# Optimization experiments

Measured on AMD Instinct MI355X. Metric: run time of the kernel, lower is better.

The kernel has to match this reference:

```python
import jax, jax.numpy as jnp
import numpy as np

N_NODES = 100000
N_EDGES = 1600000
N_FEAT = 64
HIDDEN = 16


def setup_inputs() -> dict:
    key = jax.random.key(0)
    ks = jax.random.split(key, 10)
    x = jax.random.normal(ks[0], (N_NODES, N_FEAT), dtype=jnp.float32)
    edge_index = jax.random.randint(ks[1], (2, N_EDGES), 0, N_NODES, dtype=jnp.int64)
    As = jax.random.normal(ks[2], (2, N_EDGES), dtype=jnp.float32)
    ws_weights = jax.random.normal(ks[3], (2,), dtype=jnp.float32)
    Wl1 = jax.random.normal(ks[4], (N_FEAT, HIDDEN), dtype=jnp.float32) / np.sqrt(N_FEAT)
    bl1 = jnp.zeros((HIDDEN,), dtype=jnp.float32)
    Wr1 = jax.random.normal(ks[5], (N_FEAT, HIDDEN), dtype=jnp.float32) / np.sqrt(N_FEAT)
    Wl2 = jax.random.normal(ks[6], (HIDDEN, 1), dtype=jnp.float32) / np.sqrt(HIDDEN)
    bl2 = jnp.zeros((1,), dtype=jnp.float32)
    Wr2 = jax.random.normal(ks[7], (HIDDEN, 1), dtype=jnp.float32) / np.sqrt(HIDDEN)
    return {"x": x, "edge_index": edge_index, "As": As, "ws_weights": ws_weights,
            "Wl1": Wl1, "bl1": bl1, "Wr1": Wr1, "Wl2": Wl2, "bl2": bl2, "Wr2": Wr2}


def reference(x, edge_index, As, ws_weights, Wl1, bl1, Wr1, Wl2, bl2, Wr2):
    # WeightedSumLayer: weighted sum of per-edge weight vectors
    ewm = jnp.einsum('m,me->e', ws_weights, As)  # [E]
    # edge mask (nonzero weighted sum keeps the edge); instead of slicing to a
    # data-dependent edge count, zero out masked messages (same aggregation).
    mask = (ewm != 0).astype(x.dtype)  # [E]
    src, dst = edge_index[0], edge_index[1]
    n = x.shape[0]

    # SAGEConv layer 1 (aggr='sum'): out = lin_l(sum_j x_j) + lin_r(x)
    msg1 = x[src] * mask[:, None]                             # [E, F]
    agg1 = jax.ops.segment_sum(msg1, dst, num_segments=n)     # [N, F]
    h = jax.nn.relu(agg1 @ Wl1 + bl1 + x @ Wr1)               # [N, H]

    # SAGEConv layer 2
    msg2 = h[src] * mask[:, None]                             # [E, H]
    agg2 = jax.ops.segment_sum(msg2, dst, num_segments=n)     # [N, H]
    out = agg2 @ Wl2 + bl2 + h @ Wr2                          # [N, 1]
    return out
```

## Files before the change

### kernel.cpp

```cpp
#include <hip/hip_runtime.h>
#include <hip/hip_bf16.h>

constexpr int NN = 100000;
constexpr int NE = 1600000;
constexpr int NF = 64;
constexpr int NH = 16;

constexpr int NPB  = 128;
constexpr int LB   = 7;
constexpr int NBKT = (NN + NPB - 1) / NPB;
constexpr int CAP  = 2560;
constexpr int TB   = 512;
constexpr int CHUNK = 8192;
constexpr int NBF   = (NE + CHUNK - 1) / CHUNK;
constexpr int NBLK_K1 = (NN + TB - 1) / TB;
constexpr int FD = NBKT + 1;

constexpr int SMEM_BYTES = CHUNK * 2 + NBKT * 4 + FD * 4 + TB * 4;

__device__ __forceinline__ float bf16_to_f32(unsigned short u) {
    return __uint_as_float(((unsigned int)u) << 16);
}
__device__ __forceinline__ unsigned short f32_to_bf16(float f) {
    __hip_bfloat16 hb = __float2bfloat16(f);
    return *reinterpret_cast<unsigned short*>(&hb);
}

__global__ __launch_bounds__(TB)
void k_fused(const float* __restrict__ x,
             const float* __restrict__ Wl1,
             const float* __restrict__ Wr1,
             unsigned short* __restrict__ p,
             float* __restrict__ r,
             const int* __restrict__ ei, const float* __restrict__ As,
             const float* __restrict__ ws,
             unsigned int* __restrict__ gchunk, int* __restrict__ fdir)
{
    __shared__ __align__(16) char smem[SMEM_BYTES];
    int role = blockIdx.x & 1;
    int rb   = blockIdx.x >> 1;
    int tid  = threadIdx.x;

    if (role == 0) {
        float* sW = (float*)smem;
        for (int i = tid; i < NF * NH; i += TB) {
            sW[i]           = Wl1[i];
            sW[NF * NH + i] = Wr1[i];
        }
        __syncthreads();

        int n = rb * TB + tid;
        if (n >= NN) return;

        float aL[NH], aR[NH];
#pragma unroll
        for (int j = 0; j < NH; ++j) { aL[j] = 0.f; aR[j] = 0.f; }

        const float4* xr = reinterpret_cast<const float4*>(x + (size_t)n * NF);
#pragma unroll
        for (int k4 = 0; k4 < NF / 4; ++k4) {
            float4 v = xr[k4];
            float xs[4] = {v.x, v.y, v.z, v.w};
#pragma unroll
            for (int t2 = 0; t2 < 4; ++t2) {
                const float* wl = &sW[(k4 * 4 + t2) * NH];
                const float* wr = &sW[NF * NH + (k4 * 4 + t2) * NH];
#pragma unroll
                for (int j = 0; j < NH; ++j) {
                    aL[j] = fmaf(xs[t2], wl[j], aL[j]);
                    aR[j] = fmaf(xs[t2], wr[j], aR[j]);
                }
            }
        }

        unsigned int pu[8];
#pragma unroll
        for (int j2 = 0; j2 < 8; ++j2)
            pu[j2] = (unsigned int)f32_to_bf16(aL[2*j2]) |
                     ((unsigned int)f32_to_bf16(aL[2*j2+1]) << 16);
        uint4* pp = reinterpret_cast<uint4*>(p + (size_t)n * NH);
        pp[0] = make_uint4(pu[0], pu[1], pu[2], pu[3]);
        pp[1] = make_uint4(pu[4], pu[5], pu[6], pu[7]);

        float4* rp = reinterpret_cast<float4*>(r + (size_t)n * NH);
#pragma unroll
        for (int j4 = 0; j4 < NH / 4; ++j4)
            rp[j4] = make_float4(aR[j4*4], aR[j4*4+1], aR[j4*4+2], aR[j4*4+3]);
    } else {
        unsigned short* srk  = (unsigned short*)smem;
        int* lcnt  = (int*)(smem + CHUNK * 2);
        int* fscan = lcnt + NBKT;
        int* tscan = fscan + FD;

        for (int i = tid; i < NBKT; i += TB) lcnt[i] = 0;
        __syncthreads();

        int base = rb * CHUNK;
        float w0 = ws[0], w1 = ws[1];

#pragma unroll
        for (int j = 0; j < CHUNK / TB; ++j) {
            int idx = j * TB + tid;
            int e = base + idx;
            unsigned short rk = 0xFFFFu;
            if (e < NE) {
                float ewm = w0 * As[e] + w1 * As[NE + e];
                if (ewm != 0.f)
                    rk = (unsigned short)atomicAdd(&lcnt[ei[NE + e] >> LB], 1);
            }
            srk[idx] = rk;
        }
        __syncthreads();

        {
            int loc[2]; int s = 0;
#pragma unroll
            for (int g = 0; g < 2; ++g) {
                int idx = tid * 2 + g;
                int v = (idx < NBKT) ? lcnt[idx] : 0;
                loc[g] = s; s += v;
            }
            tscan[tid] = s;
            __syncthreads();
            for (int off = 1; off < TB; off <<= 1) {
                int u = (tid >= off) ? tscan[tid - off] : 0;
                __syncthreads();
                tscan[tid] += u;
                __syncthreads();
            }
            int bse = (tid > 0) ? tscan[tid - 1] : 0;
#pragma unroll
            for (int g = 0; g < 2; ++g) {
                int idx = tid * 2 + g;
                if (idx < NBKT) fscan[idx] = bse + loc[g];
            }
            if (tid == TB - 1) fscan[NBKT] = tscan[TB - 1];
        }
        __syncthreads();

        for (int i = tid; i < FD; i += TB)
            fdir[(size_t)rb * FD + i] = fscan[i];

#pragma unroll
        for (int j = 0; j < CHUNK / TB; ++j) {
            int idx = j * TB + tid;
            unsigned short rk = srk[idx];
            if (rk != 0xFFFFu) {
                int e   = base + idx;
                int dst = ei[NE + e];
                int bk  = dst >> LB;
                gchunk[(size_t)rb * CHUNK + fscan[bk] + rk] =
                    ((unsigned)ei[e] << LB) | (unsigned)(dst & (NPB - 1));
            }
        }
    }
}

__global__ __launch_bounds__(256)
void k_agg1(const int* __restrict__ fdir, const unsigned int* __restrict__ gchunk,
            unsigned int* __restrict__ bmem,
            const unsigned short* __restrict__ p, const float* __restrict__ r,
            const float* __restrict__ bl1, const float* __restrict__ Wl2,
            const float* __restrict__ bl2, const float* __restrict__ Wr2,
            float* __restrict__ q, float* __restrict__ out,
            int* __restrict__ gsoff)
{
    __shared__ unsigned int sbm[CAP];
    __shared__ unsigned int ssorted[CAP];
    __shared__ int fstart[NBF];
    __shared__ int foff[NBF + 1];
    __shared__ int tscan[256];
    __shared__ int hist[NPB];
    __shared__ int hscan[NPB];
    __shared__ int soff[NPB + 1];

    int b = blockIdx.x;
    int tid = threadIdx.x;
    if (tid < NPB) hist[tid] = 0;

    {
        int sz = 0;
        if (tid < NBF) {
            int s0 = fdir[(size_t)tid * FD + b];
            int s1 = fdir[(size_t)tid * FD + b + 1];
            fstart[tid] = s0;
            sz = s1 - s0;
        }
        tscan[tid] = sz;
        __syncthreads();
        for (int off = 1; off < 256; off <<= 1) {
            int u = (tid >= off) ? tscan[tid - off] : 0;
            __syncthreads();
            tscan[tid] += u;
            __syncthreads();
        }
        if (tid < NBF) foff[tid] = tscan[tid] - sz;
        if (tid == 255) foff[NBF] = tscan[255];
    }
    __syncthreads();

    int cnt = min(foff[NBF], CAP);

    {
        int grp = tid >> 4, k = tid & 15;
        for (int f = grp; f < NBF; f += 16) {
            int o  = foff[f];
            int sz = foff[f + 1] - o;
            int s  = fstart[f];
            const unsigned int* src = gchunk + (size_t)f * CHUNK + s;
            int lim = min(sz, CAP - o);
            for (int j = k; j < lim; j += 16)
                sbm[o + j] = src[j];
        }
    }
    __syncthreads();

    int rk[CAP / 256];
#pragma unroll
    for (int j = 0; j < CAP / 256; ++j) {
        int i = j * 256 + tid;
        if (i < cnt)
            rk[j] = atomicAdd(&hist[sbm[i] & (NPB - 1)], 1);
    }
    __syncthreads();

    if (tid < NPB) hscan[tid] = hist[tid];
    __syncthreads();
    for (int off = 1; off < NPB; off <<= 1) {
        int u = (tid < NPB && tid >= off) ? hscan[tid - off] : 0;
        __syncthreads();
        if (tid < NPB) hscan[tid] += u;
        __syncthreads();
    }
    if (tid < NPB) soff[tid + 1] = hscan[tid];
    if (tid == 0) soff[0] = 0;
    __syncthreads();

#pragma unroll
    for (int j = 0; j < CAP / 256; ++j) {
        int i = j * 256 + tid;
        if (i < cnt) {
            unsigned int w = sbm[i];
            ssorted[soff[w & (NPB - 1)] + rk[j]] = w;
        }
    }
    __syncthreads();

    for (int i = tid; i < cnt; i += 256)
        bmem[(size_t)b * CAP + i] = ssorted[i];
    if (tid < NPB + 1)
        gsoff[(size_t)b * (NPB + 1) + tid] = soff[tid];

    int g = tid >> 4, k = tid & 15;
    int n0 = b * NPB;
#pragma unroll
    for (int jj = 0; jj < 8; ++jj) {
        int nl = g * 8 + jj;
        int s = soff[nl], e = soff[nl + 1];
        float a = 0.f;
        int i = s;
        for (; i + 3 < e; i += 4) {
            unsigned w0 = ssorted[i], w1 = ssorted[i+1], w2 = ssorted[i+2], w3 = ssorted[i+3];
            float v0 = bf16_to_f32(p[(size_t)(w0 >> LB) * NH + k]);
            float v1 = bf16_to_f32(p[(size_t)(w1 >> LB) * NH + k]);
            float v2 = bf16_to_f32(p[(size_t)(w2 >> LB) * NH + k]);
            float v3 = bf16_to_f32(p[(size_t)(w3 >> LB) * NH + k]);
            a += (v0 + v1) + (v2 + v3);
        }
        for (; i < e; ++i)
            a += bf16_to_f32(p[(size_t)(ssorted[i] >> LB) * NH + k]);

        int n = n0 + nl;
        if (n < NN) {
            float h = a + r[(size_t)n * NH + k] + bl1[k];
            h = h > 0.f ? h : 0.f;
            float qv = h * Wl2[k];
            float sv = h * Wr2[k];
#pragma unroll
            for (int m = 8; m >= 1; m >>= 1) {
                qv += __shfl_xor(qv, m);
                sv += __shfl_xor(sv, m);
            }
            if (k == 0) {
                q[n]   = qv;
                out[n] = sv + bl2[0];
            }
        }
    }
}

__global__ __launch_bounds__(256)
void k_agg2(const int* __restrict__ gsoff, const unsigned int* __restrict__ bmem,
            const float* __restrict__ q, float* __restrict__ out)
{
    int n = blockIdx.x * 256 + threadIdx.x;
    if (n >= NN) return;
    int b  = n >> LB;
    int dl = n & (NPB - 1);
    int s = gsoff[(size_t)b * (NPB + 1) + dl];
    int e = gsoff[(size_t)b * (NPB + 1) + dl + 1];
    const unsigned int* bm = bmem + (size_t)b * CAP;

    float a = 0.f;
    int i = s;
    for (; i + 3 < e; i += 4) {
        unsigned w0 = bm[i], w1 = bm[i+1], w2 = bm[i+2], w3 = bm[i+3];
        a += (q[w0 >> LB] + q[w1 >> LB]) + (q[w2 >> LB] + q[w3 >> LB]);
    }
    for (; i < e; ++i)
        a += q[bm[i] >> LB];
    out[n] += a;
}

extern "C" void kernel_launch(void* const* d_in, const int* in_sizes, int n_in,
                              void* d_out, int out_size, void* d_ws, size_t ws_size,
                              hipStream_t stream)
{
    const float* x   = (const float*)d_in[0];
    const int*   ei  = (const int*)  d_in[1];
    const float* As  = (const float*)d_in[2];
    const float* ws  = (const float*)d_in[3];
    const float* Wl1 = (const float*)d_in[4];
    const float* bl1 = (const float*)d_in[5];
    const float* Wr1 = (const float*)d_in[6];
    const float* Wl2 = (const float*)d_in[7];
    const float* bl2 = (const float*)d_in[8];
    const float* Wr2 = (const float*)d_in[9];
    float* out = (float*)d_out;

    unsigned short* p      = (unsigned short*)d_ws;
    float*          r      = (float*)(p + (size_t)NN * NH);
    float*          q      = r + (size_t)NN * NH;
    int*            gsoff  = (int*)(q + NN);
    int*            fdir   = gsoff + (size_t)NBKT * (NPB + 1);
    unsigned int*   gchunk = (unsigned int*)(fdir + (size_t)NBF * FD);
    unsigned int*   bmem   = gchunk + (size_t)NBF * CHUNK;

    int nblk = 2 * ((NBF > NBLK_K1) ? NBF : NBLK_K1);
    k_fused<<<nblk, TB, 0, stream>>>(x, Wl1, Wr1, p, r, ei, As, ws, gchunk, fdir);
    k_agg1<<<NBKT, 256, 0, stream>>>(fdir, gchunk, bmem, p, r, bl1, Wl2, bl2, Wr2,
                                     q, out, gsoff);
    k_agg2<<<(NN + 255) / 256, 256, 0, stream>>>(gsoff, bmem, q, out);
}
```

Baseline: 176.0 us.

## Split projection across half-blocks, use wave-shuffle scan, and spread layer-2 gather

The node-projection role of the fused kernel now has each half of a block handle one of the two weight matrices (Wl1 or Wr1) for 256 nodes. This halves per-thread accumulators and raises parallelism. The bucket prefix scan replaces a shared-memory Hillis-Steele loop, which needed many barriers, with wave-level shuffle scans plus a small per-wave sum array. The layer-2 aggregation assigns four threads per node with a shuffle reduction, so short neighbour lists are gathered with more memory parallelism. The costs are more blocks and threads launched and some idle lanes for low-degree nodes.

```diff
diff --git a/kernel.cpp b/kernel.cpp
--- a/kernel.cpp
+++ b/kernel.cpp
@@ -13,10 +13,10 @@
 constexpr int TB   = 512;
 constexpr int CHUNK = 8192;
 constexpr int NBF   = (NE + CHUNK - 1) / CHUNK;
-constexpr int NBLK_K1 = (NN + TB - 1) / TB;
+constexpr int NBG   = (NN + 255) / 256;
 constexpr int FD = NBKT + 1;
 
-constexpr int SMEM_BYTES = CHUNK * 2 + NBKT * 4 + FD * 4 + TB * 4;
+constexpr int SMEM_BYTES = CHUNK * 2 + NBKT * 4 + FD * 4 + 32;
 
 __device__ __forceinline__ float bf16_to_f32(unsigned short u) {
     return __uint_as_float(((unsigned int)u) << 16);
@@ -37,8 +37,10 @@
              unsigned int* __restrict__ gchunk, int* __restrict__ fdir)
 {
     __shared__ __align__(16) char smem[SMEM_BYTES];
-    int role = blockIdx.x & 1;
-    int rb   = blockIdx.x >> 1;
+    int m3  = blockIdx.x % 3;
+    int d3  = blockIdx.x / 3;
+    int role = (m3 == 2);
+    int rb   = role ? d3 : d3 * 2 + m3;
     int tid  = threadIdx.x;
 
     if (role == 0) {
@@ -49,12 +51,15 @@
         }
         __syncthreads();
 
-        int n = rb * TB + tid;
+        int half = tid >> 8;
+        int ln   = tid & 255;
+        int n = rb * 256 + ln;
         if (n >= NN) return;
 
-        float aL[NH], aR[NH];
-#pragma unroll
-        for (int j = 0; j < NH; ++j) { aL[j] = 0.f; aR[j] = 0.f; }
+        const float* W = sW + half * (NF * NH);
+        float acc[NH];
+#pragma unroll
+        for (int j = 0; j < NH; ++j) acc[j] = 0.f;
 
         const float4* xr = reinterpret_cast<const float4*>(x + (size_t)n * NF);
 #pragma unroll
@@ -63,34 +68,33 @@
             float xs[4] = {v.x, v.y, v.z, v.w};
 #pragma unroll
             for (int t2 = 0; t2 < 4; ++t2) {
-                const float* wl = &sW[(k4 * 4 + t2) * NH];
-                const float* wr = &sW[NF * NH + (k4 * 4 + t2) * NH];
-#pragma unroll
-                for (int j = 0; j < NH; ++j) {
-                    aL[j] = fmaf(xs[t2], wl[j], aL[j]);
-                    aR[j] = fmaf(xs[t2], wr[j], aR[j]);
-                }
-            }
-        }
-
-        unsigned int pu[8];
-#pragma unroll
-        for (int j2 = 0; j2 < 8; ++j2)
-            pu[j2] = (unsigned int)f32_to_bf16(aL[2*j2]) |
-                     ((unsigned int)f32_to_bf16(aL[2*j2+1]) << 16);
-        uint4* pp = reinterpret_cast<uint4*>(p + (size_t)n * NH);
-        pp[0] = make_uint4(pu[0], pu[1], pu[2], pu[3]);
-        pp[1] = make_uint4(pu[4], pu[5], pu[6], pu[7]);
-
-        float4* rp = reinterpret_cast<float4*>(r + (size_t)n * NH);
-#pragma unroll
-        for (int j4 = 0; j4 < NH / 4; ++j4)
-            rp[j4] = make_float4(aR[j4*4], aR[j4*4+1], aR[j4*4+2], aR[j4*4+3]);
+                const float* wrow = &W[(k4 * 4 + t2) * NH];
+#pragma unroll
+                for (int j = 0; j < NH; ++j)
+                    acc[j] = fmaf(xs[t2], wrow[j], acc[j]);
+            }
+        }
+
+        if (half == 0) {
+            unsigned int pu[8];
+#pragma unroll
+            for (int j2 = 0; j2 < 8; ++j2)
+                pu[j2] = (unsigned int)f32_to_bf16(acc[2*j2]) |
+                         ((unsigned int)f32_to_bf16(acc[2*j2+1]) << 16);
+            uint4* pp = reinterpret_cast<uint4*>(p + (size_t)n * NH);
+            pp[0] = make_uint4(pu[0], pu[1], pu[2], pu[3]);
+            pp[1] = make_uint4(pu[4], pu[5], pu[6], pu[7]);
+        } else {
+            float4* rp = reinterpret_cast<float4*>(r + (size_t)n * NH);
+#pragma unroll
+            for (int j4 = 0; j4 < NH / 4; ++j4)
+                rp[j4] = make_float4(acc[j4*4], acc[j4*4+1], acc[j4*4+2], acc[j4*4+3]);
+        }
     } else {
         unsigned short* srk  = (unsigned short*)smem;
         int* lcnt  = (int*)(smem + CHUNK * 2);
         int* fscan = lcnt + NBKT;
-        int* tscan = fscan + FD;
+        int* wsum  = fscan + FD;
 
         for (int i = tid; i < NBKT; i += TB) lcnt[i] = 0;
         __syncthreads();
@@ -113,28 +117,31 @@
         __syncthreads();
 
         {
-            int loc[2]; int s = 0;
+            int loc[2]; int s0 = 0;
 #pragma unroll
             for (int g = 0; g < 2; ++g) {
                 int idx = tid * 2 + g;
                 int v = (idx < NBKT) ? lcnt[idx] : 0;
-                loc[g] = s; s += v;
-            }
-            tscan[tid] = s;
+                loc[g] = s0; s0 += v;
+            }
+            int lane = tid & 63, w = tid >> 6;
+            int si = s0;
+#pragma unroll
+            for (int off = 1; off < 64; off <<= 1) {
+                int u = __shfl_up(si, off);
+                if (lane >= off) si += u;
+            }
+            if (lane == 63) wsum[w] = si;
             __syncthreads();
-            for (int off = 1; off < TB; off <<= 1) {
-                int u = (tid >= off) ? tscan[tid - off] : 0;
-                __syncthreads();
-                tscan[tid] += u;
-                __syncthreads();
-            }
-            int bse = (tid > 0) ? tscan[tid - 1] : 0;
+            int bse = 0;
+            for (int i = 0; i < w; ++i) bse += wsum[i];
+            int excl = bse + si - s0;
 #pragma unroll
             for (int g = 0; g < 2; ++g) {
                 int idx = tid * 2 + g;
-                if (idx < NBKT) fscan[idx] = bse + loc[g];
-            }
-            if (tid == TB - 1) fscan[NBKT] = tscan[TB - 1];
+                if (idx < NBKT) fscan[idx] = excl + loc[g];
+            }
+            if (tid == TB - 1) fscan[NBKT] = bse + si;
         }
         __syncthreads();
 
@@ -293,7 +300,9 @@
 void k_agg2(const int* __restrict__ gsoff, const unsigned int* __restrict__ bmem,
             const float* __restrict__ q, float* __restrict__ out)
 {
-    int n = blockIdx.x * 256 + threadIdx.x;
+    int t = blockIdx.x * 256 + threadIdx.x;
+    int n = t >> 2;
+    int sub = t & 3;
     if (n >= NN) return;
     int b  = n >> LB;
     int dl = n & (NPB - 1);
@@ -302,14 +311,11 @@
     const unsigned int* bm = bmem + (size_t)b * CAP;
 
     float a = 0.f;
-    int i = s;
-    for (; i + 3 < e; i += 4) {
-        unsigned w0 = bm[i], w1 = bm[i+1], w2 = bm[i+2], w3 = bm[i+3];
-        a += (q[w0 >> LB] + q[w1 >> LB]) + (q[w2 >> LB] + q[w3 >> LB]);
-    }
-    for (; i < e; ++i)
+    for (int i = s + sub; i < e; i += 4)
         a += q[bm[i] >> LB];
-    out[n] += a;
+    a += __shfl_xor(a, 1);
+    a += __shfl_xor(a, 2);
+    if (sub == 0) out[n] += a;
 }
 
 extern "C" void kernel_launch(void* const* d_in, const int* in_sizes, int n_in,
@@ -336,9 +342,9 @@
     unsigned int*   gchunk = (unsigned int*)(fdir + (size_t)NBF * FD);
     unsigned int*   bmem   = gchunk + (size_t)NBF * CHUNK;
 
-    int nblk = 2 * ((NBF > NBLK_K1) ? NBF : NBLK_K1);
+    int nblk = 3 * NBF;
     k_fused<<<nblk, TB, 0, stream>>>(x, Wl1, Wr1, p, r, ei, As, ws, gchunk, fdir);
     k_agg1<<<NBKT, 256, 0, stream>>>(fdir, gchunk, bmem, p, r, bl1, Wl2, bl2, Wr2,
                                      q, out, gsoff);
-    k_agg2<<<(NN + 255) / 256, 256, 0, stream>>>(gsoff, bmem, q, out);
-}
+    k_agg2<<<(NN * 4 + 255) / 256, 256, 0, stream>>>(gsoff, bmem, q, out);
+}
```

After: 174.6 us. No clear change (-0.8%).
